# Performance work log

Hardware: AMD Instinct MI355X
Metric: run time of the kernel (lower is better)

Reference implementation:

```python
import jax, jax.numpy as jnp
import numpy as np

KK = 9  # 3x3 kernel taps
BN_EPS = 1e-5


def setup_inputs() -> dict:
    key = jax.random.key(0)
    ks = jax.random.split(key, 8)
    B, C, H, W = 2, 64, 256, 256
    O = 64
    x = jax.random.normal(ks[0], (B, C, H, W), dtype=jnp.float32)
    # offset/mask conv: 3*KK output channels (dy[9], dx[9], mask[9])
    w_off = jax.random.normal(ks[1], (3 * KK, C, 3, 3), dtype=jnp.float32) * 0.05
    b_off = jnp.zeros((3 * KK,), dtype=jnp.float32)
    # deformable conv weight
    w = jax.random.normal(ks[2], (O, C, 3, 3), dtype=jnp.float32) * (1.0 / np.sqrt(C * KK))
    b = jnp.zeros((O,), dtype=jnp.float32)
    gamma = jnp.ones((O,), dtype=jnp.float32)
    beta = jnp.zeros((O,), dtype=jnp.float32)
    return {"x": x, "w_off": w_off, "b_off": b_off, "w": w, "b": b,
            "gamma": gamma, "beta": beta}


def _dcn_bn_act_res(x, w_off, b_off, w, b, gamma, beta):
    B, C, H, W = x.shape
    O = w.shape[0]
    # offset/mask prediction via plain 3x3 conv
    om = jax.lax.conv_general_dilated(
        x, w_off, window_strides=(1, 1), padding=[(1, 1), (1, 1)],
        dimension_numbers=("NCHW", "OIHW", "NCHW")) + b_off[None, :, None, None]
    off_y = om[:, :KK]            # [B,9,H,W]
    off_x = om[:, KK:2 * KK]      # [B,9,H,W]
    mask = jax.nn.sigmoid(om[:, 2 * KK:])  # [B,9,H,W] modulation

    # absolute sampling coordinates: base grid + kernel tap offset (-1..1) + learned offset
    ky, kx = jnp.meshgrid(jnp.arange(3), jnp.arange(3), indexing="ij")
    ky = ky.reshape(KK).astype(jnp.float32) - 1.0
    kx = kx.reshape(KK).astype(jnp.float32) - 1.0
    hs = jnp.arange(H, dtype=jnp.float32)
    ws = jnp.arange(W, dtype=jnp.float32)
    py = off_y + hs[None, None, :, None] + ky[None, :, None, None]  # [B,9,H,W]
    px = off_x + ws[None, None, None, :] + kx[None, :, None, None]

    y0 = jnp.floor(py)
    x0 = jnp.floor(px)
    wy = py - y0
    wx = px - x0
    y0i = y0.astype(jnp.int32)
    x0i = x0.astype(jnp.int32)

    def gather(img, yi, xi):
        # img [C,H,W], yi/xi [9,H,W]; zero outside (implicit zero padding)
        valid = (yi >= 0) & (yi < H) & (xi >= 0) & (xi < W)
        yc = jnp.clip(yi, 0, H - 1)
        xc = jnp.clip(xi, 0, W - 1)
        return img[:, yc, xc] * valid[None].astype(img.dtype)  # [C,9,H,W]

    def sample_one(img, yi, xi, wy_, wx_):
        v00 = gather(img, yi, xi)
        v01 = gather(img, yi, xi + 1)
        v10 = gather(img, yi + 1, xi)
        v11 = gather(img, yi + 1, xi + 1)
        w00 = ((1 - wy_) * (1 - wx_))[None]
        w01 = ((1 - wy_) * wx_)[None]
        w10 = (wy_ * (1 - wx_))[None]
        w11 = (wy_ * wx_)[None]
        return v00 * w00 + v01 * w01 + v10 * w10 + v11 * w11  # [C,9,H,W]

    sampled = jax.vmap(sample_one)(x, y0i, x0i, wy, wx)  # [B,C,9,H,W]
    sampled = sampled * mask[:, None]

    out = jnp.einsum("bckhw,ock->bohw", sampled, w.reshape(O, C, KK))
    out = out + b[None, :, None, None]

    # BatchNorm (training-mode batch statistics)
    mu = out.mean(axis=(0, 2, 3), keepdims=True)
    var = out.var(axis=(0, 2, 3), keepdims=True)
    out = (out - mu) * jax.lax.rsqrt(var + BN_EPS)
    out = out * gamma[None, :, None, None] + beta[None, :, None, None]

    return jax.nn.relu(out) + x  # residual


def reference(x, w_off, b_off, w, b, gamma, beta):
    return _dcn_bn_act_res(x, w_off, b_off, w, b, gamma, beta)
```

## Files before the change

### kernel.cpp

```cpp
#include <hip/hip_runtime.h>
#include <hip/hip_fp16.h>
#include <math.h>

#define HWSZ 65536
#define IMGH 256
#define IMGW 256

typedef _Float16 half8 __attribute__((ext_vector_type(8)));
typedef float f32x4 __attribute__((ext_vector_type(4)));

__device__ inline unsigned short f2bf(float f) {
    unsigned u = __float_as_uint(f);
    return (unsigned short)((u + 0x7fffu + ((u >> 16) & 1u)) >> 16);
}
__device__ inline unsigned short f2h(float f) {
    __half h = __float2half(f);
    return __half_as_ushort(h);
}
__device__ inline __half2 duph2(unsigned s) {
    union { unsigned u; __half2 h; } c;
    c.u = (s & 0xffffu) * 0x10001u;
    return c.h;
}
__device__ inline void hacc(const uint4& q, __half2 w, __half2* v) {
    const __half2* h = (const __half2*)&q;
    v[0] = __hfma2(h[0], w, v[0]);
    v[1] = __hfma2(h[1], w, v[1]);
    v[2] = __hfma2(h[2], w, v[2]);
    v[3] = __hfma2(h[3], w, v[3]);
}

__global__ void prep_weights(const float* __restrict__ w_off,
                             const float* __restrict__ w,
                             unsigned short* __restrict__ wApack,
                             unsigned short* __restrict__ wOffPack) {
    int i = blockIdx.x * 256 + threadIdx.x;
    if (i < 36864) {
        int e = i;
        int j = e & 7, lane = (e >> 3) & 63, kk = (e >> 9) & 1;
        int t2 = e >> 10;
        int tap = t2 % 9, g = t2 / 9;
        int o = g * 16 + (lane & 15);
        int c = kk * 32 + ((lane >> 4) & 3) * 8 + j;
        wApack[e] = f2h(w[(o * 64 + c) * 9 + tap]);
    } else if (i < 36864 + 18432) {
        int e = i - 36864;
        int j = e & 7, lane = (e >> 3) & 63, kk = (e >> 9) & 1;
        int t2 = e >> 10;
        int tap = t2 % 9, mt = t2 / 9;
        int d = mt * 16 + (lane & 15);
        int c = kk * 32 + ((lane >> 4) & 3) * 8 + j;
        float v = (d < 27) ? w_off[(d * 64 + c) * 9 + tap] : 0.f;
        wOffPack[e] = f2h(v);
    }
}

__global__ __launch_bounds__(256) void transpose_x(const float* __restrict__ x,
                                                   unsigned short* __restrict__ xT) {
    __shared__ float tile[64 * 65];
    int blk = blockIdx.x;
    int b = blk >> 10;
    int p0 = (blk & 1023) * 64;
    int t = threadIdx.x;
    const float* xb = x + (size_t)b * 64 * HWSZ;
    unsigned short* xTb = xT + (size_t)b * HWSZ * 64;
    int pp = t & 63;
    int c0r = t >> 6;
#pragma unroll
    for (int i = 0; i < 16; ++i) {
        int c = c0r + 4 * i;
        tile[c * 65 + pp] = xb[(size_t)c * HWSZ + p0 + pp];
    }
    __syncthreads();
#pragma unroll
    for (int it = 0; it < 2; ++it) {
        int item = t + it * 256;
        int p = item >> 3;
        int c0 = (item & 7) * 8;
        uint4 ow;
        ow.x = f2h(tile[(c0 + 0) * 65 + p]) | ((unsigned)f2h(tile[(c0 + 1) * 65 + p]) << 16);
        ow.y = f2h(tile[(c0 + 2) * 65 + p]) | ((unsigned)f2h(tile[(c0 + 3) * 65 + p]) << 16);
        ow.z = f2h(tile[(c0 + 4) * 65 + p]) | ((unsigned)f2h(tile[(c0 + 5) * 65 + p]) << 16);
        ow.w = f2h(tile[(c0 + 6) * 65 + p]) | ((unsigned)f2h(tile[(c0 + 7) * 65 + p]) << 16);
        *(uint4*)&xTb[(size_t)(p0 + p) * 64 + c0] = ow;
    }
}

__global__ __launch_bounds__(512, 4) void dcn_main(const unsigned short* __restrict__ xT,
                                                   const unsigned short* __restrict__ wApack,
                                                   const unsigned short* __restrict__ wOffPack,
                                                   const float* __restrict__ b_off,
                                                   unsigned short* __restrict__ preout,
                                                   float* __restrict__ stats) {
    __shared__ uint4 haloBuf[3744];
    __shared__ float om_s[27 * 128];
    __shared__ float bstats[128];
    char* halo = (char*)haloBuf;
    unsigned* prmi = (unsigned*)om_s;
    uint2* prmw_s = (uint2*)(om_s + 1152);
    int bid = blockIdx.x;
    int blk = ((bid & 7) << 7) | (bid >> 3);
    int b = blk >> 9;
    int tb = blk & 511;
    int ty = tb >> 5, tx = tb & 31;
    int h0 = ty * 16, w0 = tx * 8;
    int t = threadIdx.x;
    const char* xbb = (const char*)(xT + (size_t)b * HWSZ * 64);
    int lane = t & 63;
    int wid = t >> 6;
    int lp = lane & 15;
    int lhi = lane >> 4;
    unsigned lhi16 = (unsigned)(lhi << 4);
    int p = wid * 16 + lp;
    int hb = h0 - 5, wb = w0 - 5;

    if (t < 128) bstats[t] = 0.f;

    for (int i = t; i < 3744; i += 512) {
        int cell = i >> 3;
        int ch = i & 7;
        int r = cell / 18, c = cell - r * 18;
        int y = hb + r, xx = wb + c;
        uint4 v = {0u, 0u, 0u, 0u};
        if ((unsigned)y < 256u && (unsigned)xx < 256u)
            v = *(const uint4*)(xbb + ((size_t)((y << 8) + xx) << 7) + (ch << 4));
        *(uint4*)(halo + (cell << 7) + ((ch ^ (cell & 7)) << 4)) = v;
    }
    __syncthreads();

    {
        int mt = wid & 1;
        const half8* wp = (const half8*)wOffPack;
        f32x4 z0 = {0.f, 0.f, 0.f, 0.f};
#pragma unroll
        for (int hf = 0; hf < 2; ++hf) {
            int nt = (wid >> 1) + hf * 4;
            int pp = nt * 16 + lp;
            int pr = pp >> 3, pc = pp & 7;
            f32x4 oa = z0;
#pragma unroll
            for (int tap = 0; tap < 9; ++tap) {
                int dy = tap / 3, dx = tap - dy * 3;
                int cell = (pr + dy + 4) * 18 + (pc + dx + 4);
                unsigned ad = (((unsigned)cell << 7) | (((unsigned)cell & 7) << 4)) ^ lhi16;
                half8 b0 = *(const half8*)(halo + ad);
                half8 b1 = *(const half8*)(halo + (ad ^ 64u));
                half8 wa0 = wp[((mt * 9 + tap) * 2 + 0) * 64 + lane];
                half8 wa1 = wp[((mt * 9 + tap) * 2 + 1) * 64 + lane];
                oa = __builtin_amdgcn_mfma_f32_16x16x32_f16(wa0, b0, oa, 0, 0, 0);
                oa = __builtin_amdgcn_mfma_f32_16x16x32_f16(wa1, b1, oa, 0, 0, 0);
            }
#pragma unroll
            for (int jj = 0; jj < 4; ++jj) {
                int d = mt * 16 + lhi * 4 + jj;
                if (d < 27) om_s[d * 128 + pp] = oa[jj] + b_off[d];
            }
        }
    }
    __syncthreads();

#define PARAMS(I, EOUT, WOUT)                                                 \
    {                                                                         \
        int i_ = (I);                                                         \
        int tp_ = i_ >> 7, pp_ = i_ & 127;                                    \
        int hh_ = h0 + (pp_ >> 3), wc_ = w0 + (pp_ & 7);                      \
        float offy = om_s[tp_ * 128 + pp_];                                   \
        float offx = om_s[(tp_ + 9) * 128 + pp_];                             \
        float mraw = om_s[(tp_ + 18) * 128 + pp_];                            \
        float m_ = 1.f / (1.f + __expf(-mraw));                               \
        float pyf = (float)(hh_ + tp_ / 3 - 1) + offy;                        \
        float pxf = (float)(wc_ + tp_ % 3 - 1) + offx;                        \
        float y0f = floorf(pyf), x0f = floorf(pxf);                           \
        float wy = pyf - y0f, wx = pxf - x0f;                                 \
        int y0_ = (int)y0f, x0_ = (int)x0f;                                   \
        int y1_ = y0_ + 1, x1_ = x0_ + 1;                                     \
        float vy0 = (y0_ >= 0 && y0_ < IMGH) ? 1.f : 0.f;                     \
        float vy1 = (y1_ >= 0 && y1_ < IMGH) ? 1.f : 0.f;                     \
        float vx0 = (x0_ >= 0 && x0_ < IMGW) ? 1.f : 0.f;                     \
        float vx1 = (x1_ >= 0 && x1_ < IMGW) ? 1.f : 0.f;                     \
        float w00 = (1.f - wy) * (1.f - wx) * m_ * vy0 * vx0;                 \
        float w01 = (1.f - wy) * wx * m_ * vy0 * vx1;                         \
        float w10 = wy * (1.f - wx) * m_ * vy1 * vx0;                         \
        float w11 = wy * wx * m_ * vy1 * vx1;                                 \
        WOUT = make_uint2((unsigned)f2h(w00) | ((unsigned)f2h(w01) << 16),    \
                          (unsigned)f2h(w10) | ((unsigned)f2h(w11) << 16));   \
        int ry0 = y0_ - hb, rx0 = x0_ - wb;                                   \
        if ((unsigned)ry0 <= 24u && (unsigned)rx0 <= 16u) {                   \
            EOUT = (unsigned)(ry0 * 18 + rx0) << 1;                           \
        } else {                                                              \
            int y0s = min(max(y0_, -8), 383) + 8;                             \
            int x0s = min(max(x0_, -8), 383) + 8;                             \
            EOUT = 1u | ((unsigned)y0s << 1) | ((unsigned)x0s << 10);         \
        }                                                                     \
    }
    {
        unsigned pe0, pe1, pe2 = 0;
        uint2 pw0 = make_uint2(0, 0), pw1 = pw0, pw2 = pw0;
        PARAMS(t, pe0, pw0);
        PARAMS(t + 512, pe1, pw1);
        if (t < 128) PARAMS(t + 1024, pe2, pw2);
        __syncthreads();
        prmi[t] = pe0;        prmw_s[t] = pw0;
        prmi[t + 512] = pe1;  prmw_s[t + 512] = pw1;
        if (t < 128) { prmi[t + 1024] = pe2; prmw_s[t + 1024] = pw2; }
    }
#undef PARAMS
    __syncthreads();

    f32x4 z = {0.f, 0.f, 0.f, 0.f};
    f32x4 acc[4] = {z, z, z, z};
    const half8* ap = (const half8*)wApack;
    uint4 q[4][2];

#define SBASE(CC) ((((CC) << 7) | (((CC) & 7u) << 4)) ^ lhi16)
#define LOADC(E)                                                              \
    {                                                                         \
        unsigned e_ = (E);                                                    \
        bool fb_ = (e_ & 1u);                                                 \
        unsigned cl_ = fb_ ? 0u : (e_ >> 1);                                  \
        unsigned a00 = SBASE(cl_), a01 = SBASE(cl_ + 1u);                     \
        unsigned a10 = SBASE(cl_ + 18u), a11 = SBASE(cl_ + 19u);              \
        q[0][0] = *(const uint4*)(halo + a00);                                \
        q[0][1] = *(const uint4*)(halo + (a00 ^ 64u));                        \
        q[1][0] = *(const uint4*)(halo + a01);                                \
        q[1][1] = *(const uint4*)(halo + (a01 ^ 64u));                        \
        q[2][0] = *(const uint4*)(halo + a10);                                \
        q[2][1] = *(const uint4*)(halo + (a10 ^ 64u));                        \
        q[3][0] = *(const uint4*)(halo + a11);                                \
        q[3][1] = *(const uint4*)(halo + (a11 ^ 64u));                        \
        if (__ballot(fb_)) {                                                  \
            if (fb_) {                                                        \
                int y0r = (int)((e_ >> 1) & 511) - 8;                         \
                int x0r = (int)((e_ >> 10) & 511) - 8;                        \
                int y0c = min(max(y0r, 0), 255), y1c = min(max(y0r + 1, 0), 255); \
                int x0c = min(max(x0r, 0), 255), x1c = min(max(x0r + 1, 0), 255); \
                const char* g00 = xbb + (((y0c << 8) + x0c) << 7) + (lhi << 4); \
                const char* g01 = xbb + (((y0c << 8) + x1c) << 7) + (lhi << 4); \
                const char* g10 = xbb + (((y1c << 8) + x0c) << 7) + (lhi << 4); \
                const char* g11 = xbb + (((y1c << 8) + x1c) << 7) + (lhi << 4); \
                q[0][0] = *(const uint4*)g00; q[0][1] = *(const uint4*)(g00 + 64); \
                q[1][0] = *(const uint4*)g01; q[1][1] = *(const uint4*)(g01 + 64); \
                q[2][0] = *(const uint4*)g10; q[2][1] = *(const uint4*)(g10 + 64); \
                q[3][0] = *(const uint4*)g11; q[3][1] = *(const uint4*)(g11 + 64); \
            }                                                                 \
        }                                                                     \
    }

    unsigned pi = prmi[p];
    uint2 ww = prmw_s[p];
    LOADC(pi);

#pragma unroll
    for (int tap = 0; tap < 9; ++tap) {
        __half2 W00 = duph2(ww.x), W01 = duph2(ww.x >> 16);
        __half2 W10 = duph2(ww.y), W11 = duph2(ww.y >> 16);
        union HV { __half2 h2[4]; half8 h8; } V0, V1;
        __half2 z2 = __float2half2_rn(0.f);
#pragma unroll
        for (int j = 0; j < 4; ++j) { V0.h2[j] = z2; V1.h2[j] = z2; }
        hacc(q[0][0], W00, V0.h2); hacc(q[0][1], W00, V1.h2);
        hacc(q[1][0], W01, V0.h2); hacc(q[1][1], W01, V1.h2);
        hacc(q[2][0], W10, V0.h2); hacc(q[2][1], W10, V1.h2);
        hacc(q[3][0], W11, V0.h2); hacc(q[3][1], W11, V1.h2);
        half8 b0 = V0.h8, b1 = V1.h8;
        if (tap < 8) {
            pi = prmi[(tap + 1) * 128 + p];
            ww = prmw_s[(tap + 1) * 128 + p];
            LOADC(pi);
        }
        __builtin_amdgcn_s_setprio(1);
#pragma unroll
        for (int g2 = 0; g2 < 4; ++g2) {
            half8 a0 = ap[((g2 * 9 + tap) * 2 + 0) * 64 + lane];
            half8 a1 = ap[((g2 * 9 + tap) * 2 + 1) * 64 + lane];
            acc[g2] = __builtin_amdgcn_mfma_f32_16x16x32_f16(a0, b0, acc[g2], 0, 0, 0);
            acc[g2] = __builtin_amdgcn_mfma_f32_16x16x32_f16(a1, b1, acc[g2], 0, 0, 0);
        }
        __builtin_amdgcn_s_setprio(0);
    }
#undef LOADC
#undef SBASE

    unsigned short* pob = preout + (size_t)b * 64 * HWSZ;
    int gp = (h0 + (p >> 3)) * IMGW + w0 + (p & 7);
#pragma unroll
    for (int g2 = 0; g2 < 4; ++g2) {
#pragma unroll
        for (int jj = 0; jj < 4; ++jj) {
            int o = g2 * 16 + lhi * 4 + jj;
            pob[(size_t)o * HWSZ + gp] = f2bf(acc[g2][jj]);
        }
    }
#pragma unroll
    for (int g2 = 0; g2 < 4; ++g2) {
#pragma unroll
        for (int jj = 0; jj < 4; ++jj) {
            float s1 = acc[g2][jj];
            float s2 = s1 * s1;
#pragma unroll
            for (int mask = 1; mask < 16; mask <<= 1) {
                s1 += __shfl_xor(s1, mask);
                s2 += __shfl_xor(s2, mask);
            }
            if (lp == 0) {
                int o = g2 * 16 + lhi * 4 + jj;
                atomicAdd(&bstats[o], s1);
                atomicAdd(&bstats[64 + o], s2);
            }
        }
    }
    __syncthreads();
    if (t < 128) atomicAdd(&stats[t], bstats[t]);
}

__global__ __launch_bounds__(256) void bn_finalize(const float* __restrict__ stats,
                                                   const float* __restrict__ gamma,
                                                   const float* __restrict__ beta,
                                                   const float* __restrict__ x,
                                                   const unsigned short* __restrict__ preout,
                                                   float* __restrict__ out) {
    int i = blockIdx.x * 256 + threadIdx.x;
    int e0 = i * 8;
    int o = (e0 >> 16) & 63;
    const float inv_n = 1.f / 131072.f;
    float mean = stats[o] * inv_n;
    float var = stats[64 + o] * inv_n - mean * mean;
    float rstd = rsqrtf(var + 1e-5f);
    float g = gamma[o] * rstd;
    float bb = beta[o] - mean * g;
    uint4 q = ((const uint4*)preout)[i];
    float4 x0 = ((const float4*)x)[i * 2];
    float4 x1 = ((const float4*)x)[i * 2 + 1];
    float4 r0, r1;
    r0.x = fmaxf(__uint_as_float(q.x << 16) * g + bb, 0.f) + x0.x;
    r0.y = fmaxf(__uint_as_float(q.x & 0xffff0000u) * g + bb, 0.f) + x0.y;
    r0.z = fmaxf(__uint_as_float(q.y << 16) * g + bb, 0.f) + x0.z;
    r0.w = fmaxf(__uint_as_float(q.y & 0xffff0000u) * g + bb, 0.f) + x0.w;
    r1.x = fmaxf(__uint_as_float(q.z << 16) * g + bb, 0.f) + x1.x;
    r1.y = fmaxf(__uint_as_float(q.z & 0xffff0000u) * g + bb, 0.f) + x1.y;
    r1.z = fmaxf(__uint_as_float(q.w << 16) * g + bb, 0.f) + x1.z;
    r1.w = fmaxf(__uint_as_float(q.w & 0xffff0000u) * g + bb, 0.f) + x1.w;
    ((float4*)out)[i * 2] = r0;
    ((float4*)out)[i * 2 + 1] = r1;
}

extern "C" void kernel_launch(void* const* d_in, const int* in_sizes, int n_in,
                              void* d_out, int out_size, void* d_ws, size_t ws_size,
                              hipStream_t stream) {
    const float* x     = (const float*)d_in[0];
    const float* w_off = (const float*)d_in[1];
    const float* b_off = (const float*)d_in[2];
    const float* w     = (const float*)d_in[3];
    const float* gamma = (const float*)d_in[5];
    const float* beta  = (const float*)d_in[6];
    float* out = (float*)d_out;
    char* wsb = (char*)d_ws;

    unsigned short* xT       = (unsigned short*)wsb;
    unsigned short* preout   = (unsigned short*)(wsb + 16777216);
    unsigned short* wApack   = (unsigned short*)(wsb + 33554432);
    unsigned short* wOffPack = (unsigned short*)(wsb + 33628160);
    float*          stats    = (float*)(wsb + 33665024);

    hipMemsetAsync(stats, 0, 512, stream);
    prep_weights<<<216, 256, 0, stream>>>(w_off, w, wApack, wOffPack);
    transpose_x<<<2048, 256, 0, stream>>>(x, xT);
    dcn_main<<<1024, 512, 0, stream>>>(xT, wApack, wOffPack, b_off, preout, stats);
    bn_finalize<<<4096, 256, 0, stream>>>(stats, gamma, beta, x, preout, out);
}
```

Before: 93.88 us.

## Drop LDS halo tile and gather bilinear samples directly from global memory

```diff
diff --git a/kernel.cpp b/kernel.cpp
--- a/kernel.cpp
+++ b/kernel.cpp
@@ -86,16 +86,14 @@
     }
 }
 
-__global__ __launch_bounds__(512, 4) void dcn_main(const unsigned short* __restrict__ xT,
+__global__ __launch_bounds__(512, 8) void dcn_main(const unsigned short* __restrict__ xT,
                                                    const unsigned short* __restrict__ wApack,
                                                    const unsigned short* __restrict__ wOffPack,
                                                    const float* __restrict__ b_off,
                                                    unsigned short* __restrict__ preout,
                                                    float* __restrict__ stats) {
-    __shared__ uint4 haloBuf[3744];
     __shared__ float om_s[27 * 128];
     __shared__ float bstats[128];
-    char* halo = (char*)haloBuf;
     unsigned* prmi = (unsigned*)om_s;
     uint2* prmw_s = (uint2*)(om_s + 1152);
     int bid = blockIdx.x;
@@ -112,25 +110,13 @@
     int lhi = lane >> 4;
     unsigned lhi16 = (unsigned)(lhi << 4);
     int p = wid * 16 + lp;
-    int hb = h0 - 5, wb = w0 - 5;
 
     if (t < 128) bstats[t] = 0.f;
-
-    for (int i = t; i < 3744; i += 512) {
-        int cell = i >> 3;
-        int ch = i & 7;
-        int r = cell / 18, c = cell - r * 18;
-        int y = hb + r, xx = wb + c;
-        uint4 v = {0u, 0u, 0u, 0u};
-        if ((unsigned)y < 256u && (unsigned)xx < 256u)
-            v = *(const uint4*)(xbb + ((size_t)((y << 8) + xx) << 7) + (ch << 4));
-        *(uint4*)(halo + (cell << 7) + ((ch ^ (cell & 7)) << 4)) = v;
-    }
-    __syncthreads();
 
     {
         int mt = wid & 1;
         const half8* wp = (const half8*)wOffPack;
+        half8 hz = {0, 0, 0, 0, 0, 0, 0, 0};
         f32x4 z0 = {0.f, 0.f, 0.f, 0.f};
 #pragma unroll
         for (int hf = 0; hf < 2; ++hf) {
@@ -141,10 +127,11 @@
 #pragma unroll
             for (int tap = 0; tap < 9; ++tap) {
                 int dy = tap / 3, dx = tap - dy * 3;
-                int cell = (pr + dy + 4) * 18 + (pc + dx + 4);
-                unsigned ad = (((unsigned)cell << 7) | (((unsigned)cell & 7) << 4)) ^ lhi16;
-                half8 b0 = *(const half8*)(halo + ad);
-                half8 b1 = *(const half8*)(halo + (ad ^ 64u));
+                int y = h0 + pr + dy - 1, xx = w0 + pc + dx - 1;
+                bool inb = ((unsigned)y < 256u) && ((unsigned)xx < 256u);
+                const char* ga = xbb + (((size_t)((y << 8) + xx)) << 7) + lhi16;
+                half8 b0 = inb ? *(const half8*)ga : hz;
+                half8 b1 = inb ? *(const half8*)(ga + 64) : hz;
                 half8 wa0 = wp[((mt * 9 + tap) * 2 + 0) * 64 + lane];
                 half8 wa1 = wp[((mt * 9 + tap) * 2 + 1) * 64 + lane];
                 oa = __builtin_amdgcn_mfma_f32_16x16x32_f16(wa0, b0, oa, 0, 0, 0);
@@ -184,14 +171,11 @@
         float w11 = wy * wx * m_ * vy1 * vx1;                                 \
         WOUT = make_uint2((unsigned)f2h(w00) | ((unsigned)f2h(w01) << 16),    \
                           (unsigned)f2h(w10) | ((unsigned)f2h(w11) << 16));   \
-        int ry0 = y0_ - hb, rx0 = x0_ - wb;                                   \
-        if ((unsigned)ry0 <= 24u && (unsigned)rx0 <= 16u) {                   \
-            EOUT = (unsigned)(ry0 * 18 + rx0) << 1;                           \
-        } else {                                                              \
-            int y0s = min(max(y0_, -8), 383) + 8;                             \
-            int x0s = min(max(x0_, -8), 383) + 8;                             \
-            EOUT = 1u | ((unsigned)y0s << 1) | ((unsigned)x0s << 10);         \
-        }                                                                     \
+        unsigned y0c = (unsigned)min(max(y0_, 0), 255);                       \
+        unsigned y1c = (unsigned)min(max(y1_, 0), 255);                       \
+        unsigned x0c = (unsigned)min(max(x0_, 0), 255);                       \
+        unsigned x1c = (unsigned)min(max(x1_, 0), 255);                       \
+        EOUT = y0c | (y1c << 8) | (x0c << 16) | (x1c << 24);                  \
     }
     {
         unsigned pe0, pe1, pe2 = 0;
@@ -212,46 +196,26 @@
     const half8* ap = (const half8*)wApack;
     uint4 q[4][2];
 
-#define SBASE(CC) ((((CC) << 7) | (((CC) & 7u) << 4)) ^ lhi16)
 #define LOADC(E)                                                              \
     {                                                                         \
         unsigned e_ = (E);                                                    \
-        bool fb_ = (e_ & 1u);                                                 \
-        unsigned cl_ = fb_ ? 0u : (e_ >> 1);                                  \
-        unsigned a00 = SBASE(cl_), a01 = SBASE(cl_ + 1u);                     \
-        unsigned a10 = SBASE(cl_ + 18u), a11 = SBASE(cl_ + 19u);              \
-        q[0][0] = *(const uint4*)(halo + a00);                                \
-        q[0][1] = *(const uint4*)(halo + (a00 ^ 64u));                        \
-        q[1][0] = *(const uint4*)(halo + a01);                                \
-        q[1][1] = *(const uint4*)(halo + (a01 ^ 64u));                        \
-        q[2][0] = *(const uint4*)(halo + a10);                                \
-        q[2][1] = *(const uint4*)(halo + (a10 ^ 64u));                        \
-        q[3][0] = *(const uint4*)(halo + a11);                                \
-        q[3][1] = *(const uint4*)(halo + (a11 ^ 64u));                        \
-        if (__ballot(fb_)) {                                                  \
-            if (fb_) {                                                        \
-                int y0r = (int)((e_ >> 1) & 511) - 8;                         \
-                int x0r = (int)((e_ >> 10) & 511) - 8;                        \
-                int y0c = min(max(y0r, 0), 255), y1c = min(max(y0r + 1, 0), 255); \
-                int x0c = min(max(x0r, 0), 255), x1c = min(max(x0r + 1, 0), 255); \
-                const char* g00 = xbb + (((y0c << 8) + x0c) << 7) + (lhi << 4); \
-                const char* g01 = xbb + (((y0c << 8) + x1c) << 7) + (lhi << 4); \
-                const char* g10 = xbb + (((y1c << 8) + x0c) << 7) + (lhi << 4); \
-                const char* g11 = xbb + (((y1c << 8) + x1c) << 7) + (lhi << 4); \
-                q[0][0] = *(const uint4*)g00; q[0][1] = *(const uint4*)(g00 + 64); \
-                q[1][0] = *(const uint4*)g01; q[1][1] = *(const uint4*)(g01 + 64); \
-                q[2][0] = *(const uint4*)g10; q[2][1] = *(const uint4*)(g10 + 64); \
-                q[3][0] = *(const uint4*)g11; q[3][1] = *(const uint4*)(g11 + 64); \
-            }                                                                 \
-        }                                                                     \
-    }
-
-    unsigned pi = prmi[p];
-    uint2 ww = prmw_s[p];
-    LOADC(pi);
+        unsigned r0_ = (e_ & 255u) << 8, r1_ = ((e_ >> 8) & 255u) << 8;       \
+        unsigned c0_ = (e_ >> 16) & 255u, c1_ = e_ >> 24;                     \
+        const char* g00 = xbb + ((((size_t)(r0_ + c0_)) << 7) | lhi16);       \
+        const char* g01 = xbb + ((((size_t)(r0_ + c1_)) << 7) | lhi16);       \
+        const char* g10 = xbb + ((((size_t)(r1_ + c0_)) << 7) | lhi16);       \
+        const char* g11 = xbb + ((((size_t)(r1_ + c1_)) << 7) | lhi16);       \
+        q[0][0] = *(const uint4*)g00; q[0][1] = *(const uint4*)(g00 + 64);    \
+        q[1][0] = *(const uint4*)g01; q[1][1] = *(const uint4*)(g01 + 64);    \
+        q[2][0] = *(const uint4*)g10; q[2][1] = *(const uint4*)(g10 + 64);    \
+        q[3][0] = *(const uint4*)g11; q[3][1] = *(const uint4*)(g11 + 64);    \
+    }
 
 #pragma unroll
     for (int tap = 0; tap < 9; ++tap) {
+        unsigned pi = prmi[tap * 128 + p];
+        uint2 ww = prmw_s[tap * 128 + p];
+        LOADC(pi);
         __half2 W00 = duph2(ww.x), W01 = duph2(ww.x >> 16);
         __half2 W10 = duph2(ww.y), W11 = duph2(ww.y >> 16);
         union HV { __half2 h2[4]; half8 h8; } V0, V1;
@@ -263,11 +227,6 @@
         hacc(q[2][0], W10, V0.h2); hacc(q[2][1], W10, V1.h2);
         hacc(q[3][0], W11, V0.h2); hacc(q[3][1], W11, V1.h2);
         half8 b0 = V0.h8, b1 = V1.h8;
-        if (tap < 8) {
-            pi = prmi[(tap + 1) * 128 + p];
-            ww = prmw_s[(tap + 1) * 128 + p];
-            LOADC(pi);
-        }
         __builtin_amdgcn_s_setprio(1);
 #pragma unroll
         for (int g2 = 0; g2 < 4; ++g2) {
@@ -279,7 +238,6 @@
         __builtin_amdgcn_s_setprio(0);
     }
 #undef LOADC
-#undef SBASE
 
     unsigned short* pob = preout + (size_t)b * 64 * HWSZ;
     int gp = (h0 + (p >> 3)) * IMGW + w0 + (p & 7);
```

New measurement: 179.4 us. 1.91x slower.

## Split halo staging into two channel halves to halve LDS footprint

Applied to the files above, without the earlier changes.

```diff
diff --git a/kernel.cpp b/kernel.cpp
--- a/kernel.cpp
+++ b/kernel.cpp
@@ -92,7 +92,7 @@
                                                    const float* __restrict__ b_off,
                                                    unsigned short* __restrict__ preout,
                                                    float* __restrict__ stats) {
-    __shared__ uint4 haloBuf[3744];
+    __shared__ uint4 haloBuf[1872];
     __shared__ float om_s[27 * 128];
     __shared__ float bstats[128];
     char* halo = (char*)haloBuf;
@@ -116,44 +116,64 @@
 
     if (t < 128) bstats[t] = 0.f;
 
-    for (int i = t; i < 3744; i += 512) {
-        int cell = i >> 3;
-        int ch = i & 7;
-        int r = cell / 18, c = cell - r * 18;
-        int y = hb + r, xx = wb + c;
-        uint4 v = {0u, 0u, 0u, 0u};
-        if ((unsigned)y < 256u && (unsigned)xx < 256u)
-            v = *(const uint4*)(xbb + ((size_t)((y << 8) + xx) << 7) + (ch << 4));
-        *(uint4*)(halo + (cell << 7) + ((ch ^ (cell & 7)) << 4)) = v;
-    }
-    __syncthreads();
-
+#define STAGE(HS)                                                             \
+    for (int i = t; i < 1872; i += 512) {                                     \
+        int cell = i >> 2;                                                    \
+        int ch = i & 3;                                                       \
+        int r = cell / 18, c = cell - r * 18;                                 \
+        int y = hb + r, xx = wb + c;                                          \
+        uint4 v = {0u, 0u, 0u, 0u};                                           \
+        if ((unsigned)y < 256u && (unsigned)xx < 256u)                        \
+            v = *(const uint4*)(xbb + ((size_t)((y << 8) + xx) << 7)          \
+                                + (HS) * 64 + (ch << 4));                     \
+        *(uint4*)(halo + (cell << 6) + ((ch ^ (cell & 3)) << 4)) = v;         \
+    }
+
+    f32x4 zc = {0.f, 0.f, 0.f, 0.f};
+    f32x4 oa0 = zc, oa1 = zc;
+
+#define CONVH(HS)                                                             \
+    {                                                                         \
+        int mt = wid & 1;                                                     \
+        const half8* wp = (const half8*)wOffPack;                             \
+        _Pragma("unroll")                                                     \
+        for (int hf = 0; hf < 2; ++hf) {                                      \
+            int nt = (wid >> 1) + hf * 4;                                     \
+            int pp = nt * 16 + lp;                                            \
+            int pr = pp >> 3, pc = pp & 7;                                    \
+            f32x4 o_ = hf ? oa1 : oa0;                                        \
+            _Pragma("unroll")                                                 \
+            for (int tap = 0; tap < 9; ++tap) {                               \
+                int dy = tap / 3, dx = tap - dy * 3;                          \
+                int cell = (pr + dy + 4) * 18 + (pc + dx + 4);                \
+                unsigned ad = (((unsigned)cell << 6) |                        \
+                               (((unsigned)cell & 3u) << 4)) ^ lhi16;         \
+                half8 bb = *(const half8*)(halo + ad);                        \
+                half8 wa = wp[((mt * 9 + tap) * 2 + (HS)) * 64 + lane];       \
+                o_ = __builtin_amdgcn_mfma_f32_16x16x32_f16(wa, bb, o_, 0, 0, 0); \
+            }                                                                 \
+            if (hf) oa1 = o_; else oa0 = o_;                                  \
+        }                                                                     \
+    }
+
+    STAGE(0)
+    __syncthreads();
+    CONVH(0)
+    __syncthreads();
+    STAGE(1)
+    __syncthreads();
+    CONVH(1)
     {
         int mt = wid & 1;
-        const half8* wp = (const half8*)wOffPack;
-        f32x4 z0 = {0.f, 0.f, 0.f, 0.f};
 #pragma unroll
         for (int hf = 0; hf < 2; ++hf) {
             int nt = (wid >> 1) + hf * 4;
             int pp = nt * 16 + lp;
-            int pr = pp >> 3, pc = pp & 7;
-            f32x4 oa = z0;
-#pragma unroll
-            for (int tap = 0; tap < 9; ++tap) {
-                int dy = tap / 3, dx = tap - dy * 3;
-                int cell = (pr + dy + 4) * 18 + (pc + dx + 4);
-                unsigned ad = (((unsigned)cell << 7) | (((unsigned)cell & 7) << 4)) ^ lhi16;
-                half8 b0 = *(const half8*)(halo + ad);
-                half8 b1 = *(const half8*)(halo + (ad ^ 64u));
-                half8 wa0 = wp[((mt * 9 + tap) * 2 + 0) * 64 + lane];
-                half8 wa1 = wp[((mt * 9 + tap) * 2 + 1) * 64 + lane];
-                oa = __builtin_amdgcn_mfma_f32_16x16x32_f16(wa0, b0, oa, 0, 0, 0);
-                oa = __builtin_amdgcn_mfma_f32_16x16x32_f16(wa1, b1, oa, 0, 0, 0);
-            }
+            f32x4 o_ = hf ? oa1 : oa0;
 #pragma unroll
             for (int jj = 0; jj < 4; ++jj) {
                 int d = mt * 16 + lhi * 4 + jj;
-                if (d < 27) om_s[d * 128 + pp] = oa[jj] + b_off[d];
+                if (d < 27) om_s[d * 128 + pp] = o_[jj] + b_off[d];
             }
         }
     }
@@ -210,76 +230,77 @@
     f32x4 z = {0.f, 0.f, 0.f, 0.f};
     f32x4 acc[4] = {z, z, z, z};
     const half8* ap = (const half8*)wApack;
-    uint4 q[4][2];
-
-#define SBASE(CC) ((((CC) << 7) | (((CC) & 7u) << 4)) ^ lhi16)
-#define LOADC(E)                                                              \
+    uint4 q[4];
+
+#define SBASE(CC) ((((CC) << 6) | (((CC) & 3u) << 4)) ^ lhi16)
+#define LOADC(E, HS)                                                          \
     {                                                                         \
         unsigned e_ = (E);                                                    \
         bool fb_ = (e_ & 1u);                                                 \
         unsigned cl_ = fb_ ? 0u : (e_ >> 1);                                  \
         unsigned a00 = SBASE(cl_), a01 = SBASE(cl_ + 1u);                     \
         unsigned a10 = SBASE(cl_ + 18u), a11 = SBASE(cl_ + 19u);              \
-        q[0][0] = *(const uint4*)(halo + a00);                                \
-        q[0][1] = *(const uint4*)(halo + (a00 ^ 64u));                        \
-        q[1][0] = *(const uint4*)(halo + a01);                                \
-        q[1][1] = *(const uint4*)(halo + (a01 ^ 64u));                        \
-        q[2][0] = *(const uint4*)(halo + a10);                                \
-        q[2][1] = *(const uint4*)(halo + (a10 ^ 64u));                        \
-        q[3][0] = *(const uint4*)(halo + a11);                                \
-        q[3][1] = *(const uint4*)(halo + (a11 ^ 64u));                        \
+        q[0] = *(const uint4*)(halo + a00);                                   \
+        q[1] = *(const uint4*)(halo + a01);                                   \
+        q[2] = *(const uint4*)(halo + a10);                                   \
+        q[3] = *(const uint4*)(halo + a11);                                   \
         if (__ballot(fb_)) {                                                  \
             if (fb_) {                                                        \
                 int y0r = (int)((e_ >> 1) & 511) - 8;                         \
                 int x0r = (int)((e_ >> 10) & 511) - 8;                        \
                 int y0c = min(max(y0r, 0), 255), y1c = min(max(y0r + 1, 0), 255); \
                 int x0c = min(max(x0r, 0), 255), x1c = min(max(x0r + 1, 0), 255); \
-                const char* g00 = xbb + (((y0c << 8) + x0c) << 7) + (lhi << 4); \
-                const char* g01 = xbb + (((y0c << 8) + x1c) << 7) + (lhi << 4); \
-                const char* g10 = xbb + (((y1c << 8) + x0c) << 7) + (lhi << 4); \
-                const char* g11 = xbb + (((y1c << 8) + x1c) << 7) + (lhi << 4); \
-                q[0][0] = *(const uint4*)g00; q[0][1] = *(const uint4*)(g00 + 64); \
-                q[1][0] = *(const uint4*)g01; q[1][1] = *(const uint4*)(g01 + 64); \
-                q[2][0] = *(const uint4*)g10; q[2][1] = *(const uint4*)(g10 + 64); \
-                q[3][0] = *(const uint4*)g11; q[3][1] = *(const uint4*)(g11 + 64); \
+                const char* gb = xbb + (HS) * 64 + lhi16;                     \
+                q[0] = *(const uint4*)(gb + (((y0c << 8) + x0c) << 7));       \
+                q[1] = *(const uint4*)(gb + (((y0c << 8) + x1c) << 7));       \
+                q[2] = *(const uint4*)(gb + (((y1c << 8) + x0c) << 7));       \
+                q[3] = *(const uint4*)(gb + (((y1c << 8) + x1c) << 7));       \
             }                                                                 \
         }                                                                     \
     }
 
-    unsigned pi = prmi[p];
-    uint2 ww = prmw_s[p];
-    LOADC(pi);
-
-#pragma unroll
-    for (int tap = 0; tap < 9; ++tap) {
-        __half2 W00 = duph2(ww.x), W01 = duph2(ww.x >> 16);
-        __half2 W10 = duph2(ww.y), W11 = duph2(ww.y >> 16);
-        union HV { __half2 h2[4]; half8 h8; } V0, V1;
-        __half2 z2 = __float2half2_rn(0.f);
-#pragma unroll
-        for (int j = 0; j < 4; ++j) { V0.h2[j] = z2; V1.h2[j] = z2; }
-        hacc(q[0][0], W00, V0.h2); hacc(q[0][1], W00, V1.h2);
-        hacc(q[1][0], W01, V0.h2); hacc(q[1][1], W01, V1.h2);
-        hacc(q[2][0], W10, V0.h2); hacc(q[2][1], W10, V1.h2);
-        hacc(q[3][0], W11, V0.h2); hacc(q[3][1], W11, V1.h2);
-        half8 b0 = V0.h8, b1 = V1.h8;
-        if (tap < 8) {
-            pi = prmi[(tap + 1) * 128 + p];
-            ww = prmw_s[(tap + 1) * 128 + p];
-            LOADC(pi);
-        }
-        __builtin_amdgcn_s_setprio(1);
-#pragma unroll
-        for (int g2 = 0; g2 < 4; ++g2) {
-            half8 a0 = ap[((g2 * 9 + tap) * 2 + 0) * 64 + lane];
-            half8 a1 = ap[((g2 * 9 + tap) * 2 + 1) * 64 + lane];
-            acc[g2] = __builtin_amdgcn_mfma_f32_16x16x32_f16(a0, b0, acc[g2], 0, 0, 0);
-            acc[g2] = __builtin_amdgcn_mfma_f32_16x16x32_f16(a1, b1, acc[g2], 0, 0, 0);
-        }
-        __builtin_amdgcn_s_setprio(0);
-    }
+#define TAPLOOP(HS)                                                           \
+    {                                                                         \
+        unsigned pi = prmi[p];                                                \
+        uint2 ww = prmw_s[p];                                                 \
+        LOADC(pi, HS);                                                        \
+        _Pragma("unroll")                                                     \
+        for (int tap = 0; tap < 9; ++tap) {                                   \
+            __half2 W00 = duph2(ww.x), W01 = duph2(ww.x >> 16);               \
+            __half2 W10 = duph2(ww.y), W11 = duph2(ww.y >> 16);               \
+            union HV { __half2 h2[4]; half8 h8; } V0;                         \
+            __half2 z2 = __float2half2_rn(0.f);                               \
+            V0.h2[0] = z2; V0.h2[1] = z2; V0.h2[2] = z2; V0.h2[3] = z2;       \
+            hacc(q[0], W00, V0.h2);                                           \
+            hacc(q[1], W01, V0.h2);                                           \
+            hacc(q[2], W10, V0.h2);                                           \
+            hacc(q[3], W11, V0.h2);                                           \
+            half8 b0 = V0.h8;                                                 \
+            if (tap < 8) {                                                    \
+                pi = prmi[(tap + 1) * 128 + p];                               \
+                ww = prmw_s[(tap + 1) * 128 + p];                             \
+                LOADC(pi, HS);                                                \
+            }                                                                 \
+            __builtin_amdgcn_s_setprio(1);                                    \
+            _Pragma("unroll")                                                 \
+            for (int g2 = 0; g2 < 4; ++g2) {                                  \
+                half8 a0 = ap[((g2 * 9 + tap) * 2 + (HS)) * 64 + lane];       \
+                acc[g2] = __builtin_amdgcn_mfma_f32_16x16x32_f16(a0, b0, acc[g2], 0, 0, 0); \
+            }                                                                 \
+            __builtin_amdgcn_s_setprio(0);                                    \
+        }                                                                     \
+    }
+
+    TAPLOOP(1)
+    __syncthreads();
+    STAGE(0)
+    __syncthreads();
+    TAPLOOP(0)
+#undef TAPLOOP
 #undef LOADC
 #undef SBASE
+#undef CONVH
+#undef STAGE
 
     unsigned short* pob = preout + (size_t)b * 64 * HWSZ;
     int gp = (h0 + (p >> 3)) * IMGW + w0 + (p & 7);
```

New measurement: 100.2 us. 1.07x slower.
